# Optimization experiments

Measured on AMD Instinct MI355X. Metric: run time of the kernel, lower is better.

Reference implementation:

```python
import jax, jax.numpy as jnp
import numpy as np

B, T, D = 4, 8192, 512
H, BS = 8, 16


def setup_inputs() -> dict:
    key = jax.random.key(0)
    ks = jax.random.split(key, 7)
    s = 1.0 / np.sqrt(D)
    return {
        "x": jax.random.normal(ks[0], (B, T, D), dtype=jnp.float32),
        "Wq": jax.random.normal(ks[1], (D, D), dtype=jnp.float32) * s,
        "bq": jax.random.normal(ks[2], (D,), dtype=jnp.float32) * 0.02,
        "Wk": jax.random.normal(ks[3], (D, D), dtype=jnp.float32) * s,
        "bk": jax.random.normal(ks[4], (D,), dtype=jnp.float32) * 0.02,
        "Wv": jax.random.normal(ks[5], (D, D), dtype=jnp.float32) * s,
        "bv": jax.random.normal(ks[6], (D,), dtype=jnp.float32) * 0.02,
    }


def reference(x, Wq, bq, Wk, bk, Wv, bv):
    b, t, d_model = x.shape
    nb = t // BS          # number of blocks
    dh = d_model // H     # per-head dim
    # [B,T,D] -> [B,nb,BS,D] -> [B,BS,nb,D]: attention runs across blocks
    xb = x.reshape(b, nb, BS, d_model).transpose(0, 2, 1, 3)
    # projections (torch Linear: x @ W.T + b)
    q = xb @ Wq.T + bq
    k = xb @ Wk.T + bk
    v = xb @ Wv.T + bv
    # split heads: [B,BS,nb,H,dh] -> [B,BS,H,nb,dh]
    q = q.reshape(b, BS, nb, H, dh).transpose(0, 1, 3, 2, 4)
    k = k.reshape(b, BS, nb, H, dh).transpose(0, 1, 3, 2, 4)
    v = v.reshape(b, BS, nb, H, dh).transpose(0, 1, 3, 2, 4)
    scale = d_model ** (-0.5)  # note: full dim, as in the original
    attn = jnp.einsum('bshnd,bshmd->bshnm', q, k) * scale  # [B,BS,H,nb,nb]
    attn = jax.nn.softmax(attn, axis=-1)
    out = jnp.einsum('bshnm,bshmd->bshnd', attn, v)        # [B,BS,H,nb,dh]
    # merge heads and undo block permute
    out = out.transpose(0, 1, 3, 2, 4).reshape(b, BS, nb, d_model)
    out = out.transpose(0, 2, 1, 3).reshape(b, t, d_model)
    return out
```

## Files before the change

kernel.cpp:

```cpp
#include <hip/hip_runtime.h>
#include <hip/hip_bf16.h>
#include <cstdint>
#include <cstddef>

#define Bsz 4
#define Tsz 8192
#define Dsz 512
#define Hn 8
#define BSn 16
#define NBn 512
#define DHn 64
#define NQKV 1536
#define MROWS 32768

#define SCL 0.06375870136f
#define ATT_M 8.0f

typedef __attribute__((ext_vector_type(8))) short short8;
typedef __attribute__((ext_vector_type(4))) short short4v;
typedef __attribute__((ext_vector_type(4))) float float4f;

__device__ __forceinline__ uint16_t f2b(float f) {
  union { float f; uint32_t u; } v; v.f = f;
  uint32_t u = v.u;
  return (uint16_t)((u + 0x7fffu + ((u >> 16) & 1u)) >> 16);
}

__device__ __forceinline__ uint32_t pk2(float a, float b) {
  union { float f; uint32_t u; } x, y; x.f = a; y.f = b;
  return __builtin_amdgcn_perm(y.u + 0x8000u, x.u + 0x8000u, 0x07060302u);
}

__device__ __forceinline__ uint32_t pk2t(float a, float b) {
  union { float f; uint32_t u; } x, y; x.f = a; y.f = b;
  return __builtin_amdgcn_perm(y.u, x.u, 0x07060302u);
}

__device__ __forceinline__ void gl_lds16(const void* g, void* l) {
  __builtin_amdgcn_global_load_lds(
      (const __attribute__((address_space(1))) unsigned int*)g,
      (__attribute__((address_space(3))) unsigned int*)l, 16, 0, 0);
}

#define XBLK (MROWS * Dsz / 1024)
__global__ void cvt_kernel(const float* __restrict__ x, const float* __restrict__ Wq,
                           const float* __restrict__ Wk, const float* __restrict__ Wv,
                           uint16_t* __restrict__ xb, uint16_t* __restrict__ wc) {
  int bid = blockIdx.x;
  if (bid < XBLK) {
    int i = (bid * 256 + threadIdx.x) * 4;
    float4 v = *(const float4*)(x + i);
    uint64_t o = (uint64_t)pk2(v.x, v.y) | ((uint64_t)pk2(v.z, v.w) << 32);
    *(uint64_t*)(xb + i) = o;
  } else {
    int i = ((bid - XBLK) * 256 + threadIdx.x) * 4;
    int row = i >> 9;
    int col = i & 511;
    const float* src = (row < 512) ? Wq : ((row < 1024) ? Wk : Wv);
    float4 v = *(const float4*)(src + (size_t)(row & 511) * 512 + col);
    uint64_t o = (uint64_t)pk2(v.x, v.y) | ((uint64_t)pk2(v.z, v.w) << 32);
    *(uint64_t*)(wc + i) = o;
  }
}

#define BM 128
#define BN 128
#define BK 64

__global__ __launch_bounds__(256, 4) void gemm_qkv(
    const uint16_t* __restrict__ Xb, const uint16_t* __restrict__ Wc,
    const float* __restrict__ bq, const float* __restrict__ bkp,
    const float* __restrict__ bv, uint16_t* __restrict__ Qp,
    uint16_t* __restrict__ Kp, uint16_t* __restrict__ Vtmp) {
  __shared__ uint16_t As[BM * BK];
  __shared__ uint16_t Bs[BN * BK];
  const int tid = threadIdx.x;
  const int wave = tid >> 6, lane = tid & 63;
  const int lrow = lane & 15, quad = lane >> 4;

  int g = blockIdx.x;
  int xcd = g & 7, ii = g >> 3;
  int mt = xcd * 32 + ii / 12;
  int nt = ii - (ii / 12) * 12;
  const int m0 = mt * BM;
  const int n0 = nt * BN;
  const int wm = (wave >> 1) * 64, wn = (wave & 1) * 64;

  float4f acc[4][4] = {};

  for (int k0 = 0; k0 < Dsz; k0 += BK) {
    __syncthreads();
#pragma unroll
    for (int p = 0; p < 4; ++p) {
      int cbase = p * 256 + wave * 64;
      int c = cbase + lane;
      int row = c >> 3, pos = c & 7;
      int kc = (pos ^ (row & 7)) * 8;
      gl_lds16(Xb + (size_t)(m0 + row) * Dsz + k0 + kc, As + cbase * 8);
    }
#pragma unroll
    for (int p = 0; p < 4; ++p) {
      int cbase = p * 256 + wave * 64;
      int c = cbase + lane;
      int row = c >> 3, pos = c & 7;
      int kc = (pos ^ (row & 7)) * 8;
      gl_lds16(Wc + (size_t)(n0 + row) * Dsz + k0 + kc, Bs + cbase * 8);
    }
    __syncthreads();

#pragma unroll
    for (int h = 0; h < 2; ++h) {
      short8 af[4], bf[4];
#pragma unroll
      for (int i = 0; i < 4; ++i) {
        int rowA = wm + i * 16 + lrow;
        af[i] = *(const short8*)(As + rowA * BK + (((h * 4 + quad) ^ (rowA & 7)) * 8));
      }
#pragma unroll
      for (int j = 0; j < 4; ++j) {
        int rowB = wn + j * 16 + lrow;
        bf[j] = *(const short8*)(Bs + rowB * BK + (((h * 4 + quad) ^ (rowB & 7)) * 8));
      }
#pragma unroll
      for (int i = 0; i < 4; ++i)
#pragma unroll
        for (int j = 0; j < 4; ++j)
          acc[i][j] = __builtin_amdgcn_mfma_f32_16x16x32_bf16(af[i], bf[j], acc[i][j], 0, 0, 0);
    }
  }

  const int region = n0 >> 9;
  const float* bias = (region == 0) ? bq : ((region == 1) ? bkp : bv);
  const float mult = (region == 0) ? SCL : 1.0f;
  const int bb = m0 >> 13;
  const int nbbase = ((m0 & 8191) >> 4) + (wm >> 4);
  const int nv0 = (n0 & 511) + wn;

  if (region < 2) {
    uint16_t* dst = (region == 0) ? Qp : Kp;
#pragma unroll
    for (int j = 0; j < 4; ++j) {
      int nl = nv0 + j * 16 + lrow;
      int hh = nl >> 6, dh = nl & 63;
      float bval = bias[nl];
      size_t base = (size_t)bb * 4194304 + (size_t)hh * 32768 +
                    (size_t)nbbase * 64 + dh + (size_t)(quad * 4) * 262144;
#pragma unroll
      for (int i = 0; i < 4; ++i)
#pragma unroll
        for (int r = 0; r < 4; ++r)
          dst[base + (size_t)r * 262144 + (size_t)i * 64] =
              f2b((acc[i][j][r] + bval) * mult);
    }
  } else {
#pragma unroll
    for (int j = 0; j < 4; ++j) {
      int nl = nv0 + j * 16 + lrow;
      float bval = bias[nl];
#pragma unroll
      for (int i = 0; i < 4; ++i) {
        int tok = m0 + wm + i * 16 + quad * 4;
#pragma unroll
        for (int r = 0; r < 4; ++r)
          Vtmp[(size_t)(tok + r) * 512 + nl] = f2b(acc[i][j][r] + bval);
      }
    }
  }
}

__global__ __launch_bounds__(256, 3) void attn_kernel(
    const uint16_t* __restrict__ Qp, const uint16_t* __restrict__ Kp,
    const uint16_t* __restrict__ Vtmp, float* __restrict__ out) {
  __shared__ uint16_t Ks[2][32 * 64];
  __shared__ uint16_t Vs[2][32 * 64];
  __shared__ uint16_t Ps[4][4][16 * 32];

  int bx = blockIdx.x;
  const int qh = bx & 1; bx >>= 1;
  const int h = bx & 7; bx >>= 3;
  const int s = bx & 15;
  const int b = bx >> 4;

  const int tid = threadIdx.x;
  const int w = tid >> 6, lane = tid & 63;
  const int lrow = lane & 15, quad = lane >> 4;

  const size_t sh = (((size_t)b * 16 + s) * 8 + h);
  const uint16_t* Qb = Qp + (sh << 15);
  const uint16_t* Kb = Kp + (sh << 15);

  const int e_hi = tid >> 7, dtv = (tid >> 5) & 3, qv = (tid >> 3) & 3,
            jv = (tid >> 1) & 3, hbv = tid & 1;
  const int kvv = qv * 8 + e_hi * 4 + jv;
  const uint16_t* vsrc = Vtmp + ((size_t)b * Tsz + s) * 512 +
                         (size_t)kvv * 8192 + h * 64 + dtv * 16 + hbv * 8;
  const unsigned vs_base =
      (unsigned)(uintptr_t)(__attribute__((address_space(3))) const uint16_t*)&Vs[0][0];

  short8 qB[4][2];
  const int q0 = qh * 256 + w * 64;
#pragma unroll
  for (int qs = 0; qs < 4; ++qs) {
    const uint16_t* qp = Qb + (size_t)(q0 + qs * 16 + lrow) * 64;
    qB[qs][0] = *(const short8*)(qp + quad * 8);
    qB[qs][1] = *(const short8*)(qp + 32 + quad * 8);
  }

  float4f O[4][4] = {};
  float l_acc[4] = {0.f, 0.f, 0.f, 0.f};

  const int kr = w * 8 + (lane >> 3);
  const int kcs = (lane & 7) ^ (kr & 7);

  const int sw = (lrow >> 1) & 3;
  const float4f negm = {-ATT_M, -ATT_M, -ATT_M, -ATT_M};

#define ATT_STAGE(buf, kv0_) do {                                             \
    gl_lds16(Kb + (size_t)((kv0_) + kr) * 64 + kcs * 8, &Ks[buf][w * 512]);   \
    gl_lds16(vsrc + (size_t)(kv0_) * 8192, &Vs[buf][w * 512]);                \
  } while (0)

  ATT_STAGE(0, 0);
  __syncthreads();

  for (int it = 0; it < 16; ++it) {
    const int cur = it & 1;
    if (it < 15) ATT_STAGE(cur ^ 1, (it + 1) * 32);

    {
      short8 kA[2][2];
#pragma unroll
      for (int kt = 0; kt < 2; ++kt) {
        int row = kt * 16 + lrow;
#pragma unroll
        for (int kc = 0; kc < 2; ++kc) {
          int cc = (kc * 4 + quad) ^ (row & 7);
          kA[kt][kc] = *(const short8*)(&Ks[cur][row * 64 + cc * 8]);
        }
      }
#pragma unroll
      for (int qs = 0; qs < 4; ++qs) {
        float4f c0 = negm, c1 = negm;
        __builtin_amdgcn_s_setprio(1);
        c0 = __builtin_amdgcn_mfma_f32_16x16x32_bf16(kA[0][0], qB[qs][0], c0, 0, 0, 0);
        c0 = __builtin_amdgcn_mfma_f32_16x16x32_bf16(kA[0][1], qB[qs][1], c0, 0, 0, 0);
        c1 = __builtin_amdgcn_mfma_f32_16x16x32_bf16(kA[1][0], qB[qs][0], c1, 0, 0, 0);
        c1 = __builtin_amdgcn_mfma_f32_16x16x32_bf16(kA[1][1], qB[qs][1], c1, 0, 0, 0);
        __builtin_amdgcn_s_setprio(0);

        float p00 = __builtin_amdgcn_exp2f(c0[0]);
        float p01 = __builtin_amdgcn_exp2f(c0[1]);
        float p02 = __builtin_amdgcn_exp2f(c0[2]);
        float p03 = __builtin_amdgcn_exp2f(c0[3]);
        float p10 = __builtin_amdgcn_exp2f(c1[0]);
        float p11 = __builtin_amdgcn_exp2f(c1[1]);
        float p12 = __builtin_amdgcn_exp2f(c1[2]);
        float p13 = __builtin_amdgcn_exp2f(c1[3]);
        l_acc[qs] += ((p00 + p01) + (p02 + p03)) + ((p10 + p11) + (p12 + p13));

        uint32_t d0 = pk2t(p00, p01), d1 = pk2t(p02, p03);
        uint32_t d2 = pk2t(p10, p11), d3 = pk2t(p12, p13);
        uint16_t* Psq = Ps[w][qs];
        int half = (quad & 1) * 4;
        *(uint2*)(Psq + lrow * 32 + (((quad >> 1)) ^ sw) * 8 + half) = make_uint2(d0, d1);
        *(uint2*)(Psq + lrow * 32 + ((2 + (quad >> 1)) ^ sw) * 8 + half) = make_uint2(d2, d3);
      }
    }

    {
      short4v t0, t1, t2, t3, t4, t5, t6, t7;
      unsigned vaddr = vs_base + (cur << 12) + (lane << 3);
      asm volatile(
          "ds_read_b64_tr_b16 %0, %8\n\t"
          "ds_read_b64_tr_b16 %1, %8 offset:2048\n\t"
          "ds_read_b64_tr_b16 %2, %8 offset:512\n\t"
          "ds_read_b64_tr_b16 %3, %8 offset:2560\n\t"
          "ds_read_b64_tr_b16 %4, %8 offset:1024\n\t"
          "ds_read_b64_tr_b16 %5, %8 offset:3072\n\t"
          "ds_read_b64_tr_b16 %6, %8 offset:1536\n\t"
          "ds_read_b64_tr_b16 %7, %8 offset:3584\n\t"
          "s_waitcnt lgkmcnt(0)"
          : "=&v"(t0), "=&v"(t1), "=&v"(t2), "=&v"(t3),
            "=&v"(t4), "=&v"(t5), "=&v"(t6), "=&v"(t7)
          : "v"(vaddr));
      __builtin_amdgcn_sched_barrier(0);
      short8 vA[4];
      vA[0] = __builtin_shufflevector(t0, t1, 0, 1, 2, 3, 4, 5, 6, 7);
      vA[1] = __builtin_shufflevector(t2, t3, 0, 1, 2, 3, 4, 5, 6, 7);
      vA[2] = __builtin_shufflevector(t4, t5, 0, 1, 2, 3, 4, 5, 6, 7);
      vA[3] = __builtin_shufflevector(t6, t7, 0, 1, 2, 3, 4, 5, 6, 7);
#pragma unroll
      for (int qs = 0; qs < 4; ++qs) {
        short8 pB = *(const short8*)(Ps[w][qs] + lrow * 32 + (quad ^ sw) * 8);
        __builtin_amdgcn_s_setprio(1);
#pragma unroll
        for (int dt = 0; dt < 4; ++dt)
          O[dt][qs] = __builtin_amdgcn_mfma_f32_16x16x32_bf16(vA[dt], pB, O[dt][qs], 0, 0, 0);
        __builtin_amdgcn_s_setprio(0);
      }
    }

    if (it < 15) __syncthreads();
  }
#undef ATT_STAGE

#pragma unroll
  for (int qs = 0; qs < 4; ++qs) {
    float l = l_acc[qs];
    l += __shfl_xor(l, 16);
    l += __shfl_xor(l, 32);
    float inv = 1.0f / l;
    int qg = q0 + qs * 16 + lrow;
    float* op = out + ((size_t)b * Tsz + (size_t)qg * 16 + s) * Dsz + h * 64;
#pragma unroll
    for (int dt = 0; dt < 4; ++dt) {
      float4 vv;
      vv.x = O[dt][qs][0] * inv; vv.y = O[dt][qs][1] * inv;
      vv.z = O[dt][qs][2] * inv; vv.w = O[dt][qs][3] * inv;
      *(float4*)(op + dt * 16 + quad * 4) = vv;
    }
  }
}

extern "C" void kernel_launch(void* const* d_in, const int* in_sizes, int n_in,
                              void* d_out, int out_size, void* d_ws, size_t ws_size,
                              hipStream_t stream) {
  const float* x  = (const float*)d_in[0];
  const float* Wq = (const float*)d_in[1];
  const float* bq = (const float*)d_in[2];
  const float* Wk = (const float*)d_in[3];
  const float* bk = (const float*)d_in[4];
  const float* Wv = (const float*)d_in[5];
  const float* bv = (const float*)d_in[6];
  float* out = (float*)d_out;

  uint16_t* Qp   = (uint16_t*)d_ws;
  uint16_t* Kp   = Qp + (size_t)16777216;
  uint16_t* Vtmp = Kp + (size_t)16777216;
  uint16_t* xb   = Vtmp + (size_t)16777216;
  uint16_t* wc   = xb + (size_t)16777216;

  hipLaunchKernelGGL(cvt_kernel, dim3(XBLK + NQKV * Dsz / 1024), dim3(256), 0, stream,
                     x, Wq, Wk, Wv, xb, wc);
  hipLaunchKernelGGL(gemm_qkv, dim3((MROWS / BM) * (NQKV / BN)), dim3(256), 0, stream,
                     xb, wc, bq, bk, bv, Qp, Kp, Vtmp);
  hipLaunchKernelGGL(attn_kernel, dim3(Bsz * BSn * Hn * 2), dim3(256), 0, stream,
                     Qp, Kp, Vtmp, out);
}
```

Measured before the change: 239.1 us.

## Fuse x fp32-to-bf16 conversion into QKV GEMM A-tile loads with register prefetch

Drops the separate pass that converted x to bf16 in workspace. The GEMM now reads fp32 x straight into registers, packs it to bf16 and writes the swizzled A tile to LDS itself, prefetching the next K-slice during the MFMA loop. This saves a full write and re-read of a bf16 copy of x plus part of a launch. In exchange, x is re-read in fp32 by each of the 12 N-tiles (twice the bytes of bf16), and register pressure rises.

```diff
diff --git a/kernel.cpp b/kernel.cpp
--- a/kernel.cpp
+++ b/kernel.cpp
@@ -42,25 +42,15 @@
       (__attribute__((address_space(3))) unsigned int*)l, 16, 0, 0);
 }
 
-#define XBLK (MROWS * Dsz / 1024)
-__global__ void cvt_kernel(const float* __restrict__ x, const float* __restrict__ Wq,
-                           const float* __restrict__ Wk, const float* __restrict__ Wv,
-                           uint16_t* __restrict__ xb, uint16_t* __restrict__ wc) {
-  int bid = blockIdx.x;
-  if (bid < XBLK) {
-    int i = (bid * 256 + threadIdx.x) * 4;
-    float4 v = *(const float4*)(x + i);
-    uint64_t o = (uint64_t)pk2(v.x, v.y) | ((uint64_t)pk2(v.z, v.w) << 32);
-    *(uint64_t*)(xb + i) = o;
-  } else {
-    int i = ((bid - XBLK) * 256 + threadIdx.x) * 4;
-    int row = i >> 9;
-    int col = i & 511;
-    const float* src = (row < 512) ? Wq : ((row < 1024) ? Wk : Wv);
-    float4 v = *(const float4*)(src + (size_t)(row & 511) * 512 + col);
-    uint64_t o = (uint64_t)pk2(v.x, v.y) | ((uint64_t)pk2(v.z, v.w) << 32);
-    *(uint64_t*)(wc + i) = o;
-  }
+__global__ void cvt_w(const float* __restrict__ Wq, const float* __restrict__ Wk,
+                      const float* __restrict__ Wv, uint16_t* __restrict__ wc) {
+  int i = (blockIdx.x * 256 + threadIdx.x) * 4;
+  int row = i >> 9;
+  int col = i & 511;
+  const float* src = (row < 512) ? Wq : ((row < 1024) ? Wk : Wv);
+  float4 v = *(const float4*)(src + (size_t)(row & 511) * 512 + col);
+  uint64_t o = (uint64_t)pk2(v.x, v.y) | ((uint64_t)pk2(v.z, v.w) << 32);
+  *(uint64_t*)(wc + i) = o;
 }
 
 #define BM 128
@@ -68,7 +58,7 @@
 #define BK 64
 
 __global__ __launch_bounds__(256, 4) void gemm_qkv(
-    const uint16_t* __restrict__ Xb, const uint16_t* __restrict__ Wc,
+    const float* __restrict__ Xf, const uint16_t* __restrict__ Wc,
     const float* __restrict__ bq, const float* __restrict__ bkp,
     const float* __restrict__ bv, uint16_t* __restrict__ Qp,
     uint16_t* __restrict__ Kp, uint16_t* __restrict__ Vtmp) {
@@ -86,17 +76,30 @@
   const int n0 = nt * BN;
   const int wm = (wave >> 1) * 64, wn = (wave & 1) * 64;
 
+  const int arow = tid >> 3;
+  const int apos = tid & 7;
+  const float* axp = Xf + (size_t)(m0 + arow) * Dsz + apos * 8;
+
+  float4 pre[4][2];
+#pragma unroll
+  for (int p = 0; p < 4; ++p) {
+    pre[p][0] = *(const float4*)(axp + (size_t)p * 32 * Dsz);
+    pre[p][1] = *(const float4*)(axp + (size_t)p * 32 * Dsz + 4);
+  }
+
   float4f acc[4][4] = {};
 
   for (int k0 = 0; k0 < Dsz; k0 += BK) {
     __syncthreads();
 #pragma unroll
     for (int p = 0; p < 4; ++p) {
-      int cbase = p * 256 + wave * 64;
-      int c = cbase + lane;
-      int row = c >> 3, pos = c & 7;
-      int kc = (pos ^ (row & 7)) * 8;
-      gl_lds16(Xb + (size_t)(m0 + row) * Dsz + k0 + kc, As + cbase * 8);
+      int row = p * 32 + arow;
+      uint4 wv;
+      wv.x = pk2(pre[p][0].x, pre[p][0].y);
+      wv.y = pk2(pre[p][0].z, pre[p][0].w);
+      wv.z = pk2(pre[p][1].x, pre[p][1].y);
+      wv.w = pk2(pre[p][1].z, pre[p][1].w);
+      *(uint4*)(As + row * BK + ((apos ^ (row & 7)) * 8)) = wv;
     }
 #pragma unroll
     for (int p = 0; p < 4; ++p) {
@@ -107,6 +110,14 @@
       gl_lds16(Wc + (size_t)(n0 + row) * Dsz + k0 + kc, Bs + cbase * 8);
     }
     __syncthreads();
+
+    if (k0 + BK < Dsz) {
+#pragma unroll
+      for (int p = 0; p < 4; ++p) {
+        pre[p][0] = *(const float4*)(axp + (size_t)p * 32 * Dsz + k0 + BK);
+        pre[p][1] = *(const float4*)(axp + (size_t)p * 32 * Dsz + k0 + BK + 4);
+      }
+    }
 
 #pragma unroll
     for (int h = 0; h < 2; ++h) {
@@ -337,13 +348,12 @@
   uint16_t* Qp   = (uint16_t*)d_ws;
   uint16_t* Kp   = Qp + (size_t)16777216;
   uint16_t* Vtmp = Kp + (size_t)16777216;
-  uint16_t* xb   = Vtmp + (size_t)16777216;
-  uint16_t* wc   = xb + (size_t)16777216;
-
-  hipLaunchKernelGGL(cvt_kernel, dim3(XBLK + NQKV * Dsz / 1024), dim3(256), 0, stream,
-                     x, Wq, Wk, Wv, xb, wc);
+  uint16_t* wc   = Vtmp + (size_t)16777216;
+
+  hipLaunchKernelGGL(cvt_w, dim3(NQKV * Dsz / 1024), dim3(256), 0, stream,
+                     Wq, Wk, Wv, wc);
   hipLaunchKernelGGL(gemm_qkv, dim3((MROWS / BM) * (NQKV / BN)), dim3(256), 0, stream,
-                     xb, wc, bq, bk, bv, Qp, Kp, Vtmp);
+                     x, wc, bq, bk, bv, Qp, Kp, Vtmp);
   hipLaunchKernelGGL(attn_kernel, dim3(Bsz * BSn * Hn * 2), dim3(256), 0, stream,
                      Qp, Kp, Vtmp, out);
 }
```

New measurement: 364.7 us. 1.53x slower.
